# Optimization experiments

Measured on AMD Instinct MI355X. Metric: run time of the kernel, lower is better.

The kernel has to match this reference:

```python
import jax, jax.numpy as jnp
import numpy as np

B, S, E, H, HID, V = 2, 1024, 1024, 8, 2048, 32000
DK = E // H
EPS = 1e-15


def _pos_encoding(seq_len, d_model, n=10000.0):
    k = np.arange(seq_len, dtype=np.float32)[:, None]
    i2 = np.arange(0, d_model, 2, dtype=np.float32)
    ang = k / (n ** (i2 / d_model))
    pe = np.zeros((seq_len, d_model), dtype=np.float32)
    pe[:, 0::2] = np.sin(ang)
    pe[:, 1::2] = np.cos(ang)
    return jnp.asarray(pe)


def setup_inputs() -> dict:
    key = jax.random.key(0)
    ks = jax.random.split(key, 16)
    std = 0.02
    inp = {
        "src": jax.random.randint(ks[0], (B, S), 0, V),
        "trg": jax.random.randint(ks[1], (B, S), 0, V),
        "emb_enc": jax.random.normal(ks[2], (V, E), jnp.float32) * std,
        "emb_dec": jax.random.normal(ks[3], (V, E), jnp.float32) * std,
        "pos": _pos_encoding(S, E),
        # 3 attention blocks (enc self, dec masked self, dec cross); each has
        # w_q, w_k, w_v, w_out stacked on axis 1 (stored as [in, out]).
        "mha_w": jax.random.normal(ks[4], (3, 4, E, E), jnp.float32) * std,
        "mha_b": jnp.zeros((3, 4, E), jnp.float32),
        # 2 FFN blocks (encoder ff1, decoder ff2)
        "ffn_w1": jax.random.normal(ks[5], (2, E, HID), jnp.float32) * std,
        "ffn_b1": jnp.zeros((2, HID), jnp.float32),
        "ffn_w2": jax.random.normal(ks[6], (2, HID, E), jnp.float32) * std,
        "ffn_b2": jnp.zeros((2, E), jnp.float32),
        # 5 custom LayerNorms
        "norm_g": jnp.ones((5, E), jnp.float32),
        "norm_b": jnp.zeros((5, E), jnp.float32),
        "wout_w": jax.random.normal(ks[7], (E, V), jnp.float32) * std,
        "wout_b": jnp.zeros((V,), jnp.float32),
    }
    return inp


def _layer_norm(x, g, b):
    m = jnp.mean(x, axis=-1, keepdims=True)
    v = jnp.mean(jnp.square(x - m), axis=-1, keepdims=True)  # biased var
    return g * (x - m) * jax.lax.rsqrt(v + EPS) + b


def _mha(x, y, w, b, causal):
    # x: queries source, y: keys/values source; w: [4,E,E], b: [4,E]
    q = (x @ w[0] + b[0]).reshape(B, S, H, DK).transpose(0, 2, 1, 3)
    k = (y @ w[1] + b[1]).reshape(B, S, H, DK).transpose(0, 2, 1, 3)
    v = (y @ w[2] + b[2]).reshape(B, S, H, DK).transpose(0, 2, 1, 3)
    scores = jnp.einsum("bhqd,bhkd->bhqk", q, k) / jnp.sqrt(jnp.float32(DK))
    if causal:
        mask = jnp.triu(jnp.ones((S, S), bool), k=1)
        scores = jnp.where(mask, -jnp.inf, scores)
    probs = jax.nn.softmax(scores, axis=-1)
    out = jnp.einsum("bhqk,bhkd->bhqd", probs, v)
    out = out.transpose(0, 2, 1, 3).reshape(B, S, E)
    return out @ w[3] + b[3]


def _ffn(x, w1, b1, w2, b2):
    return jax.nn.relu(x @ w1 + b1) @ w2 + b2  # dropout is identity at eval


def reference(src, trg, emb_enc, emb_dec, pos, mha_w, mha_b, ffn_w1, ffn_b1,
              ffn_w2, ffn_b2, norm_g, norm_b, wout_w, wout_b):
    src_e = emb_enc[src] + pos
    trg_e = emb_dec[trg] + pos
    # encoder
    enc = _layer_norm(src_e + _mha(src_e, src_e, mha_w[0], mha_b[0], False),
                      norm_g[0], norm_b[0])
    enc = _layer_norm(enc + _ffn(enc, ffn_w1[0], ffn_b1[0], ffn_w2[0], ffn_b2[0]),
                      norm_g[1], norm_b[1])
    # decoder
    dec = _layer_norm(trg_e + _mha(trg_e, trg_e, mha_w[1], mha_b[1], True),
                      norm_g[2], norm_b[2])
    dec = _layer_norm(dec + _mha(dec, enc, mha_w[2], mha_b[2], False),
                      norm_g[3], norm_b[3])
    dec = _layer_norm(dec + _ffn(dec, ffn_w1[1], ffn_b1[1], ffn_w2[1], ffn_b2[1]),
                      norm_g[4], norm_b[4])
    logits = dec @ wout_w + wout_b
    return jax.nn.softmax(logits, axis=-1)
```

## Files before the change

kernel.cpp:

```cpp
#include <hip/hip_runtime.h>
#include <hip/hip_bf16.h>

#define BB 2
#define SS 1024
#define EE 1024
#define HH 8
#define DKK 128
#define HIDD 2048
#define VV 32000

typedef unsigned short u16;
typedef __attribute__((ext_vector_type(4))) float f32x4;
typedef __attribute__((ext_vector_type(8))) short s16x8;

__device__ __forceinline__ u16 f2b(float f) {
  union { float f; unsigned u; } v; v.f = f;
  unsigned r = v.u + 0x7fffu + ((v.u >> 16) & 1u);
  return (u16)(r >> 16);
}

__global__ __launch_bounds__(256) void wconv_t(const float* __restrict__ src,
    u16* __restrict__ dst, int K, int N) {
  __shared__ float tile[32][33];
  size_t zo = (size_t)blockIdx.z * K * N;
  src += zo; dst += zo;
  int n0 = blockIdx.x * 32, k0 = blockIdx.y * 32;
  int tx = threadIdx.x & 31, ty = threadIdx.x >> 5;
#pragma unroll
  for (int i = 0; i < 32; i += 8)
    tile[ty + i][tx] = src[(size_t)(k0 + ty + i) * N + n0 + tx];
  __syncthreads();
#pragma unroll
  for (int i = 0; i < 32; i += 8)
    dst[(size_t)(n0 + ty + i) * K + k0 + tx] = f2b(tile[tx][ty + i]);
}

__global__ __launch_bounds__(256) void embed_k(const int* __restrict__ idx,
    const float* __restrict__ emb, const float* __restrict__ pos,
    float* __restrict__ of, u16* __restrict__ ob) {
  int row = blockIdx.x;
  int s = row & (SS - 1);
  int t = threadIdx.x;
  int id = idx[row];
  float4 v = ((const float4*)(emb + (size_t)id * EE))[t];
  float4 p = ((const float4*)(pos + (size_t)s * EE))[t];
  v.x += p.x; v.y += p.y; v.z += p.z; v.w += p.w;
  ((float4*)(of + (size_t)row * EE))[t] = v;
  ushort4 b4; b4.x = f2b(v.x); b4.y = f2b(v.y); b4.z = f2b(v.z); b4.w = f2b(v.w);
  ((ushort4*)(ob + (size_t)row * EE))[t] = b4;
}

__device__ __forceinline__ float wsum(float v) {
#pragma unroll
  for (int o = 1; o < 64; o <<= 1) v += __shfl_xor(v, o, 64);
  return v;
}
__device__ __forceinline__ float wmax(float v) {
#pragma unroll
  for (int o = 1; o < 64; o <<= 1) v = fmaxf(v, __shfl_xor(v, o, 64));
  return v;
}
__device__ __forceinline__ float bsum(float v, float* sb) {
  v = wsum(v);
  __syncthreads();
  if ((threadIdx.x & 63) == 0) sb[threadIdx.x >> 6] = v;
  __syncthreads();
  return sb[0] + sb[1] + sb[2] + sb[3];
}
__device__ __forceinline__ float bmax(float v, float* sb) {
  v = wmax(v);
  __syncthreads();
  if ((threadIdx.x & 63) == 0) sb[threadIdx.x >> 6] = v;
  __syncthreads();
  return fmaxf(fmaxf(sb[0], sb[1]), fmaxf(sb[2], sb[3]));
}

__global__ __launch_bounds__(256) void ln_k(const float* __restrict__ x,
    const float* __restrict__ g, const float* __restrict__ bta,
    float* __restrict__ of, u16* __restrict__ ob) {
  __shared__ float sb[4];
  int row = blockIdx.x, t = threadIdx.x;
  float4 v = ((const float4*)(x + (size_t)row * EE))[t];
  float mean = bsum(v.x + v.y + v.z + v.w, sb) * (1.0f / EE);
  float dx = v.x - mean, dy = v.y - mean, dz = v.z - mean, dw = v.w - mean;
  float var = bsum(dx * dx + dy * dy + dz * dz + dw * dw, sb) * (1.0f / EE);
  float rstd = rsqrtf(var + 1e-15f);
  float4 gg = ((const float4*)g)[t];
  float4 bb = ((const float4*)bta)[t];
  float4 o;
  o.x = gg.x * dx * rstd + bb.x;
  o.y = gg.y * dy * rstd + bb.y;
  o.z = gg.z * dz * rstd + bb.z;
  o.w = gg.w * dw * rstd + bb.w;
  ((float4*)(of + (size_t)row * EE))[t] = o;
  ushort4 b4; b4.x = f2b(o.x); b4.y = f2b(o.y); b4.z = f2b(o.z); b4.w = f2b(o.w);
  ((ushort4*)(ob + (size_t)row * EE))[t] = b4;
}

__global__ __launch_bounds__(256) void smax_k(const float* __restrict__ sc,
    u16* __restrict__ pb, int causal) {
  __shared__ float sb[4];
  int row = blockIdx.x;
  int q = row & (SS - 1);
  int t = threadIdx.x;
  const float scale = 0.08838834764831845f;
  float4 v = ((const float4*)(sc + (size_t)row * SS))[t];
  int c0 = t * 4;
  bool k0 = !causal || (c0 + 0) <= q;
  bool k1 = !causal || (c0 + 1) <= q;
  bool k2 = !causal || (c0 + 2) <= q;
  bool k3 = !causal || (c0 + 3) <= q;
  float a0 = k0 ? v.x * scale : -1e30f;
  float a1 = k1 ? v.y * scale : -1e30f;
  float a2 = k2 ? v.z * scale : -1e30f;
  float a3 = k3 ? v.w * scale : -1e30f;
  float mx = bmax(fmaxf(fmaxf(a0, a1), fmaxf(a2, a3)), sb);
  float e0 = k0 ? __expf(a0 - mx) : 0.0f;
  float e1 = k1 ? __expf(a1 - mx) : 0.0f;
  float e2 = k2 ? __expf(a2 - mx) : 0.0f;
  float e3 = k3 ? __expf(a3 - mx) : 0.0f;
  float inv = 1.0f / bsum(e0 + e1 + e2 + e3, sb);
  ushort4 b4;
  b4.x = f2b(e0 * inv); b4.y = f2b(e1 * inv);
  b4.z = f2b(e2 * inv); b4.w = f2b(e3 * inv);
  ((ushort4*)(pb + (size_t)row * SS))[t] = b4;
}

__global__ __launch_bounds__(256) void vsmax_k(float* __restrict__ lg) {
  __shared__ float sb[4];
  int row = blockIdx.x, t = threadIdx.x;
  float* r = lg + (size_t)row * VV;
  float mx = -1e30f;
  for (int c = t; c < VV / 4; c += 256) {
    float4 v = ((const float4*)r)[c];
    mx = fmaxf(mx, fmaxf(fmaxf(v.x, v.y), fmaxf(v.z, v.w)));
  }
  float M = bmax(mx, sb);
  float s = 0.0f;
  for (int c = t; c < VV / 4; c += 256) {
    float4 v = ((const float4*)r)[c];
    s += __expf(v.x - M) + __expf(v.y - M) + __expf(v.z - M) + __expf(v.w - M);
  }
  float inv = 1.0f / bsum(s, sb);
  for (int c = t; c < VV / 4; c += 256) {
    float4 v = ((const float4*)r)[c];
    float4 o;
    o.x = __expf(v.x - M) * inv; o.y = __expf(v.y - M) * inv;
    o.z = __expf(v.z - M) * inv; o.w = __expf(v.w - M) * inv;
    ((float4*)r)[c] = o;
  }
}

template<bool BIAS, bool RELU, bool RES, bool WF32, bool WBF16, bool VT>
__global__ __launch_bounds__(256) void gemm_nt(
    const u16* __restrict__ A, const u16* __restrict__ Bm,
    const float* __restrict__ bias, const float* __restrict__ res,
    float* __restrict__ Cf, u16* __restrict__ Cb,
    int M, int N, int K, int lda, int ldb, int ldc,
    long long sAb, long long sAh, long long sBb, long long sBh,
    long long sCb, long long sCh) {
  (void)M; (void)N;
  int z = blockIdx.z;
  int bz = z / HH, hz = z % HH;
  A += bz * sAb + hz * sAh;
  Bm += bz * sBb + hz * sBh;
  size_t coff = (size_t)(bz * sCb + hz * sCh);

  __shared__ u16 As[128][40];
  __shared__ u16 Bs[128][40];

  int tid = threadIdx.x;
  int lane = tid & 63;
  int wave = tid >> 6;
  int wr = wave >> 1, wc = wave & 1;
  int m0 = blockIdx.y * 128, n0 = blockIdx.x * 128;
  int lrow = lane & 15;
  int lk8 = (lane >> 4) << 3;

  f32x4 acc[4][4] = {};

  for (int k0 = 0; k0 < K; k0 += 32) {
#pragma unroll
    for (int i = 0; i < 2; ++i) {
      int c = tid + i * 256;
      int r = c >> 2, c8 = (c & 3) << 3;
      uint4 va = *(const uint4*)(A + (size_t)(m0 + r) * lda + k0 + c8);
      *(uint4*)(&As[r][c8]) = va;
      uint4 vb = *(const uint4*)(Bm + (size_t)(n0 + r) * ldb + k0 + c8);
      *(uint4*)(&Bs[r][c8]) = vb;
    }
    __syncthreads();
    s16x8 af[4], bfr[4];
#pragma unroll
    for (int m = 0; m < 4; ++m)
      af[m] = *(const s16x8*)(&As[wr * 64 + m * 16 + lrow][lk8]);
#pragma unroll
    for (int n = 0; n < 4; ++n)
      bfr[n] = *(const s16x8*)(&Bs[wc * 64 + n * 16 + lrow][lk8]);
#pragma unroll
    for (int m = 0; m < 4; ++m)
#pragma unroll
      for (int n = 0; n < 4; ++n)
        acc[m][n] = __builtin_amdgcn_mfma_f32_16x16x32_bf16(af[m], bfr[n], acc[m][n], 0, 0, 0);
    __syncthreads();
  }

  int rbase = (lane >> 4) << 2;
  int cl = lane & 15;
#pragma unroll
  for (int m = 0; m < 4; ++m) {
#pragma unroll
    for (int n = 0; n < 4; ++n) {
#pragma unroll
      for (int r = 0; r < 4; ++r) {
        int row = m0 + wr * 64 + m * 16 + rbase + r;
        int col = n0 + wc * 64 + n * 16 + cl;
        float v = acc[m][n][r];
        if constexpr (BIAS) v += bias[col];
        if constexpr (RELU) v = fmaxf(v, 0.0f);
        if constexpr (RES) v += res[coff + (size_t)row * ldc + col];
        if constexpr (WF32) Cf[coff + (size_t)row * ldc + col] = v;
        if constexpr (WBF16) {
          if constexpr (VT) {
            int bb = row >> 10, sx = row & (SS - 1);
            int hh = col >> 7, dd = col & (DKK - 1);
            Cb[(((size_t)(bb * HH + hh) * DKK + dd) << 10) + sx] = f2b(v);
          } else {
            Cb[coff + (size_t)row * ldc + col] = f2b(v);
          }
        }
      }
    }
  }
}

extern "C" void kernel_launch(void* const* d_in, const int* in_sizes, int n_in,
                              void* d_out, int out_size, void* d_ws, size_t ws_size,
                              hipStream_t stream) {
  (void)in_sizes; (void)n_in; (void)out_size; (void)ws_size;
  const int* src = (const int*)d_in[0];
  const int* trg = (const int*)d_in[1];
  const float* embe = (const float*)d_in[2];
  const float* embd = (const float*)d_in[3];
  const float* pos = (const float*)d_in[4];
  const float* mha_w = (const float*)d_in[5];
  const float* mha_b = (const float*)d_in[6];
  const float* fw1 = (const float*)d_in[7];
  const float* fb1 = (const float*)d_in[8];
  const float* fw2 = (const float*)d_in[9];
  const float* fb2 = (const float*)d_in[10];
  const float* ng = (const float*)d_in[11];
  const float* nb = (const float*)d_in[12];
  const float* ww = (const float*)d_in[13];
  const float* wb = (const float*)d_in[14];
  float* out = (float*)d_out;

  char* ws = (char*)d_ws;
  size_t off = 0;
  auto alloc = [&](size_t bytes) -> void* {
    void* p = ws + off;
    off += (bytes + 255) & ~(size_t)255;
    return p;
  };

  u16* wt_mha = (u16*)alloc((size_t)12 * EE * EE * 2);
  u16* wt_f1 = (u16*)alloc((size_t)2 * EE * HIDD * 2);
  u16* wt_f2 = (u16*)alloc((size_t)2 * HIDD * EE * 2);
  u16* wt_o = (u16*)alloc((size_t)VV * EE * 2);
  float* f0 = (float*)alloc((size_t)BB * SS * EE * 4);
  float* f1 = (float*)alloc((size_t)BB * SS * EE * 4);
  float* f2 = (float*)alloc((size_t)BB * SS * EE * 4);
  float* f3 = (float*)alloc((size_t)BB * SS * EE * 4);
  u16* be = (u16*)alloc((size_t)BB * SS * EE * 2);
  u16* bd = (u16*)alloc((size_t)BB * SS * EE * 2);
  u16* qb = (u16*)alloc((size_t)BB * SS * EE * 2);
  u16* kb = (u16*)alloc((size_t)BB * SS * EE * 2);
  u16* vt = (u16*)alloc((size_t)BB * HH * DKK * SS * 2);
  u16* ao = (u16*)alloc((size_t)BB * SS * EE * 2);
  u16* hb = (u16*)alloc((size_t)BB * SS * HIDD * 2);
  u16* pb = (u16*)alloc((size_t)BB * HH * SS * SS * 2);
  float* sc = (float*)alloc((size_t)BB * HH * SS * SS * 4);

  wconv_t<<<dim3(EE / 32, EE / 32, 12), 256, 0, stream>>>(mha_w, wt_mha, EE, EE);
  wconv_t<<<dim3(HIDD / 32, EE / 32, 2), 256, 0, stream>>>(fw1, wt_f1, EE, HIDD);
  wconv_t<<<dim3(EE / 32, HIDD / 32, 2), 256, 0, stream>>>(fw2, wt_f2, HIDD, EE);
  wconv_t<<<dim3(VV / 32, EE / 32, 1), 256, 0, stream>>>(ww, wt_o, EE, VV);

  const int M = BB * SS;

  auto attn_block = [&](const u16* xq, const u16* xkv, const float* resid,
                        int blk, int causal, float* outf) {
    const u16* wq = wt_mha + (size_t)(blk * 4 + 0) * EE * EE;
    const u16* wk = wt_mha + (size_t)(blk * 4 + 1) * EE * EE;
    const u16* wv = wt_mha + (size_t)(blk * 4 + 2) * EE * EE;
    const u16* wo = wt_mha + (size_t)(blk * 4 + 3) * EE * EE;
    const float* bq = mha_b + (blk * 4 + 0) * EE;
    const float* bk = mha_b + (blk * 4 + 1) * EE;
    const float* bv = mha_b + (blk * 4 + 2) * EE;
    const float* bo = mha_b + (blk * 4 + 3) * EE;
    gemm_nt<true, false, false, false, true, false><<<dim3(8, 16, 1), 256, 0, stream>>>(
        xq, wq, bq, nullptr, nullptr, qb, M, EE, EE, EE, EE, EE, 0, 0, 0, 0, 0, 0);
    gemm_nt<true, false, false, false, true, false><<<dim3(8, 16, 1), 256, 0, stream>>>(
        xkv, wk, bk, nullptr, nullptr, kb, M, EE, EE, EE, EE, EE, 0, 0, 0, 0, 0, 0);
    gemm_nt<true, false, false, false, true, true><<<dim3(8, 16, 1), 256, 0, stream>>>(
        xkv, wv, bv, nullptr, nullptr, vt, M, EE, EE, EE, EE, EE, 0, 0, 0, 0, 0, 0);
    gemm_nt<false, false, false, true, false, false><<<dim3(8, 8, 16), 256, 0, stream>>>(
        qb, kb, nullptr, nullptr, sc, nullptr, SS, SS, DKK, EE, EE, SS,
        (long long)SS * EE, DKK, (long long)SS * EE, DKK,
        (long long)HH * SS * SS, (long long)SS * SS);
    smax_k<<<dim3(BB * HH * SS), 256, 0, stream>>>(sc, pb, causal);
    gemm_nt<false, false, false, false, true, false><<<dim3(1, 8, 16), 256, 0, stream>>>(
        pb, vt, nullptr, nullptr, nullptr, ao, SS, DKK, SS, SS, SS, EE,
        (long long)HH * SS * SS, (long long)SS * SS,
        (long long)HH * DKK * SS, (long long)DKK * SS,
        (long long)SS * EE, DKK);
    gemm_nt<true, false, true, true, false, false><<<dim3(8, 16, 1), 256, 0, stream>>>(
        ao, wo, bo, resid, outf, nullptr, M, EE, EE, EE, EE, EE, 0, 0, 0, 0, 0, 0);
  };

  auto ffn_block = [&](const u16* x, const float* resid, int blk, float* outf) {
    gemm_nt<true, true, false, false, true, false><<<dim3(16, 16, 1), 256, 0, stream>>>(
        x, wt_f1 + (size_t)blk * EE * HIDD, fb1 + blk * HIDD, nullptr, nullptr, hb,
        M, HIDD, EE, EE, EE, HIDD, 0, 0, 0, 0, 0, 0);
    gemm_nt<true, false, true, true, false, false><<<dim3(8, 16, 1), 256, 0, stream>>>(
        hb, wt_f2 + (size_t)blk * HIDD * EE, fb2 + blk * EE, resid, outf, nullptr,
        M, EE, HIDD, HIDD, HIDD, EE, 0, 0, 0, 0, 0, 0);
  };

  embed_k<<<dim3(M), 256, 0, stream>>>(src, embe, pos, f0, be);
  attn_block(be, be, f0, 0, 0, f3);
  ln_k<<<dim3(M), 256, 0, stream>>>(f3, ng + 0 * EE, nb + 0 * EE, f0, be);
  ffn_block(be, f0, 0, f3);
  ln_k<<<dim3(M), 256, 0, stream>>>(f3, ng + 1 * EE, nb + 1 * EE, f1, be);
  embed_k<<<dim3(M), 256, 0, stream>>>(trg, embd, pos, f2, bd);
  attn_block(bd, bd, f2, 1, 1, f3);
  ln_k<<<dim3(M), 256, 0, stream>>>(f3, ng + 2 * EE, nb + 2 * EE, f2, bd);
  attn_block(bd, be, f2, 2, 0, f3);
  ln_k<<<dim3(M), 256, 0, stream>>>(f3, ng + 3 * EE, nb + 3 * EE, f2, bd);
  ffn_block(bd, f2, 1, f3);
  ln_k<<<dim3(M), 256, 0, stream>>>(f3, ng + 4 * EE, nb + 4 * EE, f2, bd);
  gemm_nt<true, false, false, true, false, false><<<dim3(VV / 128, 16, 1), 256, 0, stream>>>(
      bd, wt_o, wb, nullptr, out, nullptr, M, VV, EE, EE, EE, VV, 0, 0, 0, 0, 0, 0);
  vsmax_k<<<dim3(M), 256, 0, stream>>>(out);
}
```

Measured before the change: 1.707 ms.

## Fuse QKV projections, use direct-to-LDS loads, swizzle blocks, fuse vocab softmax sum

Merges the Q/K/V projection GEMMs into one launch (or a Q launch plus a fused K/V launch for cross-attention) that scatters results into separate buffers. GEMM tiles are now loaded with global_load_lds directly into unpadded shared memory, and an XCD-aware block swizzle is added. The vocab GEMM epilogue accumulates exp(logit) row sums via atomics, so the final softmax becomes one normalization pass. That pass skips max subtraction, which risks overflow for large logits, and the unpadded LDS layout may cause bank conflicts.

After: 1.528 ms. 10.5% less time.

```diff
diff --git a/kernel.cpp b/kernel.cpp
--- a/kernel.cpp
+++ b/kernel.cpp
@@ -17,6 +17,12 @@
   union { float f; unsigned u; } v; v.f = f;
   unsigned r = v.u + 0x7fffu + ((v.u >> 16) & 1u);
   return (u16)(r >> 16);
+}
+
+typedef __attribute__((address_space(1))) const unsigned gu32;
+typedef __attribute__((address_space(3))) unsigned lu32;
+__device__ __forceinline__ void gld16(const u16* g, u16* l) {
+  __builtin_amdgcn_global_load_lds((gu32*)g, (lu32*)l, 16, 0, 0);
 }
 
 __global__ __launch_bounds__(256) void wconv_t(const float* __restrict__ src,
@@ -126,54 +132,57 @@
   ((ushort4*)(pb + (size_t)row * SS))[t] = b4;
 }
 
-__global__ __launch_bounds__(256) void vsmax_k(float* __restrict__ lg) {
-  __shared__ float sb[4];
+__global__ __launch_bounds__(256) void psmax_k(float* __restrict__ lg,
+    const float* __restrict__ rs) {
   int row = blockIdx.x, t = threadIdx.x;
-  float* r = lg + (size_t)row * VV;
-  float mx = -1e30f;
+  float inv = 1.0f / rs[row];
+  float4* p = (float4*)(lg + (size_t)row * VV);
   for (int c = t; c < VV / 4; c += 256) {
-    float4 v = ((const float4*)r)[c];
-    mx = fmaxf(mx, fmaxf(fmaxf(v.x, v.y), fmaxf(v.z, v.w)));
-  }
-  float M = bmax(mx, sb);
-  float s = 0.0f;
-  for (int c = t; c < VV / 4; c += 256) {
-    float4 v = ((const float4*)r)[c];
-    s += __expf(v.x - M) + __expf(v.y - M) + __expf(v.z - M) + __expf(v.w - M);
-  }
-  float inv = 1.0f / bsum(s, sb);
-  for (int c = t; c < VV / 4; c += 256) {
-    float4 v = ((const float4*)r)[c];
-    float4 o;
-    o.x = __expf(v.x - M) * inv; o.y = __expf(v.y - M) * inv;
-    o.z = __expf(v.z - M) * inv; o.w = __expf(v.w - M) * inv;
-    ((float4*)r)[c] = o;
-  }
-}
-
-template<bool BIAS, bool RELU, bool RES, bool WF32, bool WBF16, bool VT>
+    float4 v = p[c];
+    v.x = __expf(v.x) * inv; v.y = __expf(v.y) * inv;
+    v.z = __expf(v.z) * inv; v.w = __expf(v.w) * inv;
+    p[c] = v;
+  }
+}
+
+template<bool BIAS, bool RELU, bool RES, bool WF32, bool WBF16, bool QKV, bool SMEXP, bool SWZ>
 __global__ __launch_bounds__(256) void gemm_nt(
     const u16* __restrict__ A, const u16* __restrict__ Bm,
     const float* __restrict__ bias, const float* __restrict__ res,
     float* __restrict__ Cf, u16* __restrict__ Cb,
-    int M, int N, int K, int lda, int ldb, int ldc,
+    u16* __restrict__ Cb2, u16* __restrict__ Cb3,
+    float* __restrict__ rowsum, int qkvoff,
+    int K, int lda, int ldb, int ldc,
     long long sAb, long long sAh, long long sBb, long long sBh,
     long long sCb, long long sCh) {
-  (void)M; (void)N;
   int z = blockIdx.z;
   int bz = z / HH, hz = z % HH;
   A += bz * sAb + hz * sAh;
   Bm += bz * sBb + hz * sBh;
   size_t coff = (size_t)(bz * sCb + hz * sCh);
 
-  __shared__ u16 As[128][40];
-  __shared__ u16 Bs[128][40];
+  __shared__ __align__(16) u16 As[128 * 32];
+  __shared__ __align__(16) u16 Bs[128 * 32];
 
   int tid = threadIdx.x;
   int lane = tid & 63;
   int wave = tid >> 6;
   int wr = wave >> 1, wc = wave & 1;
-  int m0 = blockIdx.y * 128, n0 = blockIdx.x * 128;
+
+  int mi, ni;
+  if constexpr (SWZ) {
+    int nwg = gridDim.x * gridDim.y;
+    int flat = blockIdx.x + gridDim.x * blockIdx.y;
+    int q8 = nwg >> 3, r8 = nwg & 7;
+    int xcd = flat & 7, sub = flat >> 3;
+    int wg = (xcd < r8 ? xcd * (q8 + 1) : r8 * (q8 + 1) + (xcd - r8) * q8) + sub;
+    mi = wg % gridDim.y;
+    ni = wg / gridDim.y;
+  } else {
+    mi = blockIdx.y; ni = blockIdx.x;
+  }
+  int m0 = mi * 128, n0 = ni * 128;
+
   int lrow = lane & 15;
   int lk8 = (lane >> 4) << 3;
 
@@ -184,19 +193,17 @@
     for (int i = 0; i < 2; ++i) {
       int c = tid + i * 256;
       int r = c >> 2, c8 = (c & 3) << 3;
-      uint4 va = *(const uint4*)(A + (size_t)(m0 + r) * lda + k0 + c8);
-      *(uint4*)(&As[r][c8]) = va;
-      uint4 vb = *(const uint4*)(Bm + (size_t)(n0 + r) * ldb + k0 + c8);
-      *(uint4*)(&Bs[r][c8]) = vb;
+      gld16(A + (size_t)(m0 + r) * lda + k0 + c8, &As[r * 32 + c8]);
+      gld16(Bm + (size_t)(n0 + r) * ldb + k0 + c8, &Bs[r * 32 + c8]);
     }
     __syncthreads();
     s16x8 af[4], bfr[4];
 #pragma unroll
     for (int m = 0; m < 4; ++m)
-      af[m] = *(const s16x8*)(&As[wr * 64 + m * 16 + lrow][lk8]);
+      af[m] = *(const s16x8*)(&As[(wr * 64 + m * 16 + lrow) * 32 + lk8]);
 #pragma unroll
     for (int n = 0; n < 4; ++n)
-      bfr[n] = *(const s16x8*)(&Bs[wc * 64 + n * 16 + lrow][lk8]);
+      bfr[n] = *(const s16x8*)(&Bs[(wc * 64 + n * 16 + lrow) * 32 + lk8]);
 #pragma unroll
     for (int m = 0; m < 4; ++m)
 #pragma unroll
@@ -207,6 +214,7 @@
 
   int rbase = (lane >> 4) << 2;
   int cl = lane & 15;
+  float esum[4][4] = {};
 #pragma unroll
   for (int m = 0; m < 4; ++m) {
 #pragma unroll
@@ -220,17 +228,38 @@
         if constexpr (RELU) v = fmaxf(v, 0.0f);
         if constexpr (RES) v += res[coff + (size_t)row * ldc + col];
         if constexpr (WF32) Cf[coff + (size_t)row * ldc + col] = v;
-        if constexpr (WBF16) {
-          if constexpr (VT) {
+        if constexpr (SMEXP) esum[m][r] += __expf(v);
+        if constexpr (WBF16) Cb[coff + (size_t)row * ldc + col] = f2b(v);
+        if constexpr (QKV) {
+          int lcol = col + qkvoff;
+          int seg = lcol >> 10;
+          u16 bv = f2b(v);
+          if (seg == 0) {
+            Cb[(size_t)row * EE + (lcol & 1023)] = bv;
+          } else if (seg == 1) {
+            Cb2[(size_t)row * EE + (lcol & 1023)] = bv;
+          } else {
             int bb = row >> 10, sx = row & (SS - 1);
-            int hh = col >> 7, dd = col & (DKK - 1);
-            Cb[(((size_t)(bb * HH + hh) * DKK + dd) << 10) + sx] = f2b(v);
-          } else {
-            Cb[coff + (size_t)row * ldc + col] = f2b(v);
+            int h = (lcol >> 7) & 7, dd = lcol & (DKK - 1);
+            Cb3[(((size_t)(bb * HH + h) * DKK + dd) << 10) + sx] = bv;
           }
         }
       }
     }
+  }
+  if constexpr (SMEXP) {
+#pragma unroll
+    for (int m = 0; m < 4; ++m)
+#pragma unroll
+      for (int r = 0; r < 4; ++r) {
+        float p = esum[m][r];
+        p += __shfl_xor(p, 1, 64);
+        p += __shfl_xor(p, 2, 64);
+        p += __shfl_xor(p, 4, 64);
+        p += __shfl_xor(p, 8, 64);
+        if (cl == 0)
+          atomicAdd(&rowsum[m0 + wr * 64 + m * 16 + rbase + r], p);
+      }
   }
 }
 
@@ -280,6 +309,7 @@
   u16* hb = (u16*)alloc((size_t)BB * SS * HIDD * 2);
   u16* pb = (u16*)alloc((size_t)BB * HH * SS * SS * 2);
   float* sc = (float*)alloc((size_t)BB * HH * SS * SS * 4);
+  float* rsum = (float*)alloc((size_t)BB * SS * 4);
 
   wconv_t<<<dim3(EE / 32, EE / 32, 12), 256, 0, stream>>>(mha_w, wt_mha, EE, EE);
   wconv_t<<<dim3(HIDD / 32, EE / 32, 2), 256, 0, stream>>>(fw1, wt_f1, EE, HIDD);
@@ -287,44 +317,62 @@
   wconv_t<<<dim3(VV / 32, EE / 32, 1), 256, 0, stream>>>(ww, wt_o, EE, VV);
 
   const int M = BB * SS;
+  const long long Z0 = 0;
 
   auto attn_block = [&](const u16* xq, const u16* xkv, const float* resid,
                         int blk, int causal, float* outf) {
     const u16* wq = wt_mha + (size_t)(blk * 4 + 0) * EE * EE;
     const u16* wk = wt_mha + (size_t)(blk * 4 + 1) * EE * EE;
-    const u16* wv = wt_mha + (size_t)(blk * 4 + 2) * EE * EE;
     const u16* wo = wt_mha + (size_t)(blk * 4 + 3) * EE * EE;
     const float* bq = mha_b + (blk * 4 + 0) * EE;
     const float* bk = mha_b + (blk * 4 + 1) * EE;
-    const float* bv = mha_b + (blk * 4 + 2) * EE;
     const float* bo = mha_b + (blk * 4 + 3) * EE;
-    gemm_nt<true, false, false, false, true, false><<<dim3(8, 16, 1), 256, 0, stream>>>(
-        xq, wq, bq, nullptr, nullptr, qb, M, EE, EE, EE, EE, EE, 0, 0, 0, 0, 0, 0);
-    gemm_nt<true, false, false, false, true, false><<<dim3(8, 16, 1), 256, 0, stream>>>(
-        xkv, wk, bk, nullptr, nullptr, kb, M, EE, EE, EE, EE, EE, 0, 0, 0, 0, 0, 0);
-    gemm_nt<true, false, false, false, true, true><<<dim3(8, 16, 1), 256, 0, stream>>>(
-        xkv, wv, bv, nullptr, nullptr, vt, M, EE, EE, EE, EE, EE, 0, 0, 0, 0, 0, 0);
-    gemm_nt<false, false, false, true, false, false><<<dim3(8, 8, 16), 256, 0, stream>>>(
-        qb, kb, nullptr, nullptr, sc, nullptr, SS, SS, DKK, EE, EE, SS,
+    if (xq == xkv) {
+      gemm_nt<true, false, false, false, false, true, false, true>
+          <<<dim3(24, 16, 1), 256, 0, stream>>>(
+          xq, wq, bq, nullptr, nullptr, qb, kb, vt, nullptr, 0,
+          EE, EE, EE, 0, Z0, Z0, Z0, Z0, Z0, Z0);
+    } else {
+      gemm_nt<true, false, false, false, true, false, false, true>
+          <<<dim3(8, 16, 1), 256, 0, stream>>>(
+          xq, wq, bq, nullptr, nullptr, qb, nullptr, nullptr, nullptr, 0,
+          EE, EE, EE, EE, Z0, Z0, Z0, Z0, Z0, Z0);
+      gemm_nt<true, false, false, false, false, true, false, true>
+          <<<dim3(16, 16, 1), 256, 0, stream>>>(
+          xkv, wk, bk, nullptr, nullptr, qb, kb, vt, nullptr, 1024,
+          EE, EE, EE, 0, Z0, Z0, Z0, Z0, Z0, Z0);
+    }
+    gemm_nt<false, false, false, true, false, false, false, false>
+        <<<dim3(8, 8, 16), 256, 0, stream>>>(
+        qb, kb, nullptr, nullptr, sc, nullptr, nullptr, nullptr, nullptr, 0,
+        DKK, EE, EE, SS,
         (long long)SS * EE, DKK, (long long)SS * EE, DKK,
         (long long)HH * SS * SS, (long long)SS * SS);
     smax_k<<<dim3(BB * HH * SS), 256, 0, stream>>>(sc, pb, causal);
-    gemm_nt<false, false, false, false, true, false><<<dim3(1, 8, 16), 256, 0, stream>>>(
-        pb, vt, nullptr, nullptr, nullptr, ao, SS, DKK, SS, SS, SS, EE,
+    gemm_nt<false, false, false, false, true, false, false, false>
+        <<<dim3(1, 8, 16), 256, 0, stream>>>(
+        pb, vt, nullptr, nullptr, nullptr, ao, nullptr, nullptr, nullptr, 0,
+        SS, SS, SS, EE,
         (long long)HH * SS * SS, (long long)SS * SS,
         (long long)HH * DKK * SS, (long long)DKK * SS,
         (long long)SS * EE, DKK);
-    gemm_nt<true, false, true, true, false, false><<<dim3(8, 16, 1), 256, 0, stream>>>(
-        ao, wo, bo, resid, outf, nullptr, M, EE, EE, EE, EE, EE, 0, 0, 0, 0, 0, 0);
+    gemm_nt<true, false, true, true, false, false, false, true>
+        <<<dim3(8, 16, 1), 256, 0, stream>>>(
+        ao, wo, bo, resid, outf, nullptr, nullptr, nullptr, nullptr, 0,
+        EE, EE, EE, EE, Z0, Z0, Z0, Z0, Z0, Z0);
   };
 
   auto ffn_block = [&](const u16* x, const float* resid, int blk, float* outf) {
-    gemm_nt<true, true, false, false, true, false><<<dim3(16, 16, 1), 256, 0, stream>>>(
+    gemm_nt<true, true, false, false, true, false, false, true>
+        <<<dim3(16, 16, 1), 256, 0, stream>>>(
         x, wt_f1 + (size_t)blk * EE * HIDD, fb1 + blk * HIDD, nullptr, nullptr, hb,
-        M, HIDD, EE, EE, EE, HIDD, 0, 0, 0, 0, 0, 0);
-    gemm_nt<true, false, true, true, false, false><<<dim3(8, 16, 1), 256, 0, stream>>>(
+        nullptr, nullptr, nullptr, 0,
+        EE, EE, EE, HIDD, Z0, Z0, Z0, Z0, Z0, Z0);
+    gemm_nt<true, false, true, true, false, false, false, true>
+        <<<dim3(8, 16, 1), 256, 0, stream>>>(
         hb, wt_f2 + (size_t)blk * HIDD * EE, fb2 + blk * EE, resid, outf, nullptr,
-        M, EE, HIDD, HIDD, HIDD, EE, 0, 0, 0, 0, 0, 0);
+        nullptr, nullptr, nullptr, 0,
+        HIDD, HIDD, HIDD, EE, Z0, Z0, Z0, Z0, Z0, Z0);
   };
 
   embed_k<<<dim3(M), 256, 0, stream>>>(src, embe, pos, f0, be);
@@ -339,7 +387,10 @@
   ln_k<<<dim3(M), 256, 0, stream>>>(f3, ng + 3 * EE, nb + 3 * EE, f2, bd);
   ffn_block(bd, f2, 1, f3);
   ln_k<<<dim3(M), 256, 0, stream>>>(f3, ng + 4 * EE, nb + 4 * EE, f2, bd);
-  gemm_nt<true, false, false, true, false, false><<<dim3(VV / 128, 16, 1), 256, 0, stream>>>(
-      bd, wt_o, wb, nullptr, out, nullptr, M, VV, EE, EE, EE, VV, 0, 0, 0, 0, 0, 0);
-  vsmax_k<<<dim3(M), 256, 0, stream>>>(out);
-}
+  hipMemsetAsync(rsum, 0, (size_t)M * 4, stream);
+  gemm_nt<true, false, false, true, false, false, true, true>
+      <<<dim3(VV / 128, 16, 1), 256, 0, stream>>>(
+      bd, wt_o, wb, nullptr, out, nullptr, nullptr, nullptr, rsum, 0,
+      EE, EE, EE, VV, Z0, Z0, Z0, Z0, Z0, Z0);
+  psmax_k<<<dim3(M), 256, 0, stream>>>(out, rsum);
+}
```
